# Kernel tuning notes

Hardware: AMD Instinct MI355X
Metric: run time of the kernel (lower is better)

The kernel has to match this reference:

```python
import jax, jax.numpy as jnp
import numpy as np

DIM = 2048
N_HEADS = 16
N_KV = 4
HEAD_DIM = DIM // N_HEADS  # 128
G = N_HEADS // N_KV        # queries per kv head
EPS = 1e-6
ROPE_BASE = 10000.0


def _rms_norm(x, w):
    # x: [..., head_dim]
    norm = jax.lax.rsqrt(jnp.mean(x * x, axis=-1, keepdims=True) + EPS)
    return x * norm * w


def _rope_tables(seq_len, dtype):
    inv_freq = 1.0 / (ROPE_BASE ** (jnp.arange(0, HEAD_DIM, 2, dtype=jnp.float32) / HEAD_DIM))
    t = jnp.arange(seq_len, dtype=jnp.float32)
    freqs = jnp.einsum('i,j->ij', t, inv_freq)          # [S, hd/2]
    emb = jnp.concatenate([freqs, freqs], axis=-1)       # [S, hd]
    return jnp.cos(emb).astype(dtype), jnp.sin(emb).astype(dtype)


def _rotate_half(x):
    x1, x2 = x[..., : HEAD_DIM // 2], x[..., HEAD_DIM // 2:]
    return jnp.concatenate([-x2, x1], axis=-1)


def setup_inputs() -> dict:
    key = jax.random.key(0)
    ks = jax.random.split(key, 7)
    x = jax.random.normal(ks[0], (2, 2048, DIM), dtype=jnp.float32)
    s = 0.02
    Wq = jax.random.normal(ks[1], (DIM, DIM), dtype=jnp.float32) * s
    Wk = jax.random.normal(ks[2], (DIM, N_KV * HEAD_DIM), dtype=jnp.float32) * s
    Wv = jax.random.normal(ks[3], (DIM, N_KV * HEAD_DIM), dtype=jnp.float32) * s
    Wo = jax.random.normal(ks[4], (DIM, DIM), dtype=jnp.float32) * s
    q_norm_w = jnp.ones((HEAD_DIM,), dtype=jnp.float32)
    k_norm_w = jnp.ones((HEAD_DIM,), dtype=jnp.float32)
    return {"x": x, "Wq": Wq, "Wk": Wk, "Wv": Wv, "Wo": Wo,
            "q_norm_w": q_norm_w, "k_norm_w": k_norm_w}


def reference(x, Wq, Wk, Wv, Wo, q_norm_w, k_norm_w):
    B, S, _ = x.shape
    q = (x @ Wq).reshape(B, S, N_HEADS, HEAD_DIM)
    k = (x @ Wk).reshape(B, S, N_KV, HEAD_DIM)
    v = (x @ Wv).reshape(B, S, N_KV, HEAD_DIM)

    q = _rms_norm(q, q_norm_w)
    k = _rms_norm(k, k_norm_w)

    q = q.transpose(0, 2, 1, 3)  # [B, H, S, hd]
    k = k.transpose(0, 2, 1, 3)  # [B, KV, S, hd]
    v = v.transpose(0, 2, 1, 3)

    cos, sin = _rope_tables(S, x.dtype)  # [S, hd], broadcasts over B,H
    q = q * cos + _rotate_half(q) * sin
    k = k * cos + _rotate_half(k) * sin

    # GQA: group queries by kv head instead of repeating K/V (same math as repeat_interleave)
    qg = q.reshape(B, N_KV, G, S, HEAD_DIM)
    scale = HEAD_DIM ** -0.5
    scores = jnp.einsum('bkgqd,bkkd2->bkgqk2'.replace('k2', 'K').replace('d2', 'd'),
                        qg, k) if False else jnp.einsum('bkgqd,bkKd->bkgqK', qg, k) * scale
    attn = jax.nn.softmax(scores, axis=-1)               # [B, KV, G, S, S]
    out = jnp.einsum('bkgqK,bkKd->bkgqd', attn, v)       # [B, KV, G, S, hd]
    out = out.reshape(B, N_HEADS, S, HEAD_DIM).transpose(0, 2, 1, 3).reshape(B, S, DIM)
    return out @ Wo
```

## Files before the change

### kernel.cpp

```cpp
#include <hip/hip_runtime.h>
#include <stdint.h>

#define LOG2E 1.4426950408889634f

typedef __attribute__((ext_vector_type(8))) short short8;
typedef __attribute__((ext_vector_type(4))) float floatx4;
typedef unsigned int u32;

__device__ __forceinline__ float bf2f(unsigned short h) {
  union { unsigned int u; float f; } v; v.u = ((unsigned int)h) << 16; return v.f;
}
__device__ __forceinline__ unsigned short f2bf(float f) {
  union { float f; unsigned int u; } v; v.f = f;
  unsigned int r = v.u + 0x7FFFu + ((v.u >> 16) & 1u);
  return (unsigned short)(r >> 16);
}
__device__ __forceinline__ u32 fbits(float f) {
  union { float f; u32 u; } v; v.f = f; return v.u;
}
__device__ __forceinline__ void async16(void* lds, const void* g) {
  __builtin_amdgcn_global_load_lds((const __attribute__((address_space(1))) u32*)g,
                                   (__attribute__((address_space(3))) u32*)lds, 16, 0, 0);
}

__global__ __launch_bounds__(256) void cvt_f32_bf16(const float* __restrict__ src,
                                                    unsigned short* __restrict__ dst, int n) {
  int i = (blockIdx.x * 256 + threadIdx.x) * 8;
  if (i >= n) return;
  float4 a = ((const float4*)(src + i))[0];
  float4 b = ((const float4*)(src + i))[1];
  union { uint4 v; unsigned short u[8]; } o;
  o.u[0] = f2bf(a.x); o.u[1] = f2bf(a.y); o.u[2] = f2bf(a.z); o.u[3] = f2bf(a.w);
  o.u[4] = f2bf(b.x); o.u[5] = f2bf(b.y); o.u[6] = f2bf(b.z); o.u[7] = f2bf(b.w);
  *(uint4*)(dst + i) = o.v;
}

__global__ __launch_bounds__(256) void transpose_cvt4(const float* __restrict__ Wq,
                                                      const float* __restrict__ Wk,
                                                      const float* __restrict__ Wv,
                                                      const float* __restrict__ Wo,
                                                      unsigned short* __restrict__ WTqkv,
                                                      unsigned short* __restrict__ WoT) {
  const int R = 2048;
  int bid = blockIdx.x;
  const float* src; unsigned short* dst; int C;
  if (bid < 1024) { src = Wq; dst = WTqkv; C = 2048; }
  else if (bid < 1280) { src = Wk; dst = WTqkv + (size_t)2048 * 2048; C = 512; bid -= 1024; }
  else if (bid < 1536) { src = Wv; dst = WTqkv + (size_t)2048 * 2048 + (size_t)512 * 2048; C = 512; bid -= 1280; }
  else { src = Wo; dst = WoT; C = 2048; bid -= 1536; }

  __shared__ unsigned short tile[64][65];
  int tc = C >> 6;
  int br = bid / tc, bc = bid % tc;
  int r0 = br << 6, c0 = bc << 6;
  int i = threadIdx.x >> 2, cc = (threadIdx.x & 3) << 4;
  const float4* g = (const float4*)(src + (size_t)(r0 + i) * C + c0 + cc);
  float4 f0 = g[0], f1 = g[1], f2 = g[2], f3 = g[3];
  unsigned short u[16];
  u[0]=f2bf(f0.x); u[1]=f2bf(f0.y); u[2]=f2bf(f0.z); u[3]=f2bf(f0.w);
  u[4]=f2bf(f1.x); u[5]=f2bf(f1.y); u[6]=f2bf(f1.z); u[7]=f2bf(f1.w);
  u[8]=f2bf(f2.x); u[9]=f2bf(f2.y); u[10]=f2bf(f2.z); u[11]=f2bf(f2.w);
  u[12]=f2bf(f3.x); u[13]=f2bf(f3.y); u[14]=f2bf(f3.z); u[15]=f2bf(f3.w);
#pragma unroll
  for (int j = 0; j < 16; ++j) tile[i][cc + j] = u[j];
  __syncthreads();
  union { uint4 v[2]; unsigned short u[16]; } buf;
#pragma unroll
  for (int j = 0; j < 16; ++j) buf.u[j] = tile[cc + j][i];
  uint4* o = (uint4*)(dst + (size_t)(c0 + i) * R + r0 + cc);
  o[0] = buf.v[0]; o[1] = buf.v[1];
}

template <typename OutT>
__global__ __launch_bounds__(256) void gemm_nt(const unsigned short* __restrict__ A,
                                               const unsigned short* __restrict__ BT,
                                               OutT* __restrict__ C,
                                               int M, int N, int K) {
  __shared__ unsigned short As[2][128 * 32];
  __shared__ unsigned short Bs[2][128 * 32];
  const int nb = N >> 7;
  const int bm = blockIdx.x / nb, bn = blockIdx.x % nb;
  const int m0 = bm << 7, n0 = bn << 7;
  const int tid = threadIdx.x;
  const int lane = tid & 63, wave = tid >> 6;
  const int l15 = lane & 15, quad = lane >> 4;
  const int wm = (wave >> 1) << 6, wn = (wave & 1) << 6;

  floatx4 acc[4][4];
#pragma unroll
  for (int i = 0; i < 4; ++i)
#pragma unroll
    for (int j = 0; j < 4; ++j) acc[i][j] = (floatx4){0.f, 0.f, 0.f, 0.f};

  const int Lc0 = wave * 128 + lane;
#pragma unroll 1
  for (int pre = 0; pre < 1; ++pre) {
#pragma unroll
    for (int i = 0; i < 2; ++i) {
      int Lc = Lc0 + i * 64;
      int row = Lc >> 2;
      int c = (lane & 3) ^ ((row >> 1) & 3);
      async16(As[0] + (size_t)Lc * 8, A + (size_t)(m0 + row) * K + c * 8);
      async16(Bs[0] + (size_t)Lc * 8, BT + (size_t)(n0 + row) * K + c * 8);
    }
  }

  const int nk = K >> 5;
  for (int it = 0; it < nk; ++it) {
    const int cur = it & 1;
    __syncthreads();
    if (it + 1 < nk) {
      int k1 = (it + 1) << 5;
#pragma unroll
      for (int i = 0; i < 2; ++i) {
        int Lc = Lc0 + i * 64;
        int row = Lc >> 2;
        int c = (lane & 3) ^ ((row >> 1) & 3);
        async16(As[cur ^ 1] + (size_t)Lc * 8, A + (size_t)(m0 + row) * K + k1 + c * 8);
        async16(Bs[cur ^ 1] + (size_t)Lc * 8, BT + (size_t)(n0 + row) * K + k1 + c * 8);
      }
    }
    short8 af[4], bf[4];
#pragma unroll
    for (int mt = 0; mt < 4; ++mt) {
      int m = wm + mt * 16 + l15;
      af[mt] = *(const short8*)(&As[cur][(m * 4 + (quad ^ ((m >> 1) & 3))) * 8]);
    }
#pragma unroll
    for (int nt = 0; nt < 4; ++nt) {
      int n = wn + nt * 16 + l15;
      bf[nt] = *(const short8*)(&Bs[cur][(n * 4 + (quad ^ ((n >> 1) & 3))) * 8]);
    }
#pragma unroll
    for (int mt = 0; mt < 4; ++mt)
#pragma unroll
      for (int nt = 0; nt < 4; ++nt)
        acc[mt][nt] = __builtin_amdgcn_mfma_f32_16x16x32_bf16(af[mt], bf[nt], acc[mt][nt], 0, 0, 0);
  }
#pragma unroll
  for (int mt = 0; mt < 4; ++mt)
#pragma unroll
    for (int nt = 0; nt < 4; ++nt)
#pragma unroll
      for (int r = 0; r < 4; ++r) {
        int m = m0 + wm + mt * 16 + quad * 4 + r;
        int n = n0 + wn + nt * 16 + l15;
        float v = acc[mt][nt][r];
        if constexpr (sizeof(OutT) == 2)
          C[(size_t)m * N + n] = (OutT)f2bf(v);
        else
          C[(size_t)m * N + n] = (OutT)v;
      }
}

__global__ __launch_bounds__(256) void norm_rope(const unsigned short* __restrict__ qkv,
                                                 const float* __restrict__ qw,
                                                 const float* __restrict__ kw,
                                                 unsigned short* __restrict__ qT,
                                                 unsigned short* __restrict__ kT) {
  const int S = 2048;
  int wid = blockIdx.x * 4 + (threadIdx.x >> 6);
  int lane = threadIdx.x & 63;
  int slot = wid % 20;
  int bs = wid / 20;
  int s = bs & (S - 1), b = bs >> 11;
  const unsigned short* src;
  unsigned short* dst;
  const float* w;
  float scale;
  if (slot < 16) {
    src = qkv + (size_t)bs * 3072 + slot * 128;
    dst = qT + ((size_t)(b * 16 + slot) * S + s) * 128;
    w = qw; scale = 0.08838834764831845f * 1.4426950408889634f;
  } else {
    int kvi = slot - 16;
    src = qkv + (size_t)bs * 3072 + 2048 + kvi * 128;
    dst = kT + ((size_t)(b * 4 + kvi) * S + s) * 128;
    w = kw; scale = 1.0f;
  }
  float x1 = bf2f(src[lane]), x2 = bf2f(src[lane + 64]);
  float ss = x1 * x1 + x2 * x2;
#pragma unroll
  for (int m = 1; m < 64; m <<= 1) ss += __shfl_xor(ss, m, 64);
  float rms = rsqrtf(ss * (1.0f / 128.0f) + 1e-6f);
  float y1 = x1 * rms * w[lane];
  float y2 = x2 * rms * w[lane + 64];
  float ang = (float)s * exp2f((float)lane * -0.2076205059304601f);
  float c = cosf(ang), sn = sinf(ang);
  float o1 = (y1 * c - y2 * sn) * scale;
  float o2 = (y2 * c + y1 * sn) * scale;
  dst[lane] = f2bf(o1);
  dst[lane + 64] = f2bf(o2);
}

__global__ __launch_bounds__(256) void v_transpose(const unsigned short* __restrict__ qkv,
                                                   unsigned short* __restrict__ vT) {
  const int S = 2048;
  int bid = blockIdx.x;
  int dt = bid & 1, st = (bid >> 1) & 31, kv = (bid >> 6) & 3, b = bid >> 8;
  int s0 = st << 6, d0 = dt << 6;
  __shared__ unsigned short tile[64][65];
  int i = threadIdx.x >> 2, cc = (threadIdx.x & 3) << 4;
  union { uint4 v[2]; unsigned short u[16]; } buf;
  const uint4* g = (const uint4*)(qkv + ((size_t)(b * S) + s0 + i) * 3072 + 2560 + kv * 128 + d0 + cc);
  buf.v[0] = g[0]; buf.v[1] = g[1];
#pragma unroll
  for (int j = 0; j < 16; ++j) tile[i][cc + j] = buf.u[j];
  __syncthreads();
#pragma unroll
  for (int j = 0; j < 16; ++j) buf.u[j] = tile[cc + j][i];
  uint4* o = (uint4*)(vT + ((size_t)(b * 4 + kv) * 128 + d0 + i) * S + s0 + cc);
  o[0] = buf.v[0]; o[1] = buf.v[1];
}

__global__ __launch_bounds__(256, 2) void flash_attn(const unsigned short* __restrict__ qT,
                                                     const unsigned short* __restrict__ kT,
                                                     const unsigned short* __restrict__ vT,
                                                     unsigned short* __restrict__ ao) {
  const int S = 2048;
  int bid = blockIdx.x;
  int qt = bid & 15, h = (bid >> 4) & 15, b = bid >> 8;
  int kv = h >> 2;
  int tid = threadIdx.x;
  int lane = tid & 63, wave = tid >> 6;
  int l15 = lane & 15, quad = lane >> 4;

  __shared__ unsigned short Ks[2][64 * 128];
  __shared__ unsigned short VTs[2][128 * 64];
  __shared__ unsigned short Ps[4][32 * 64];
  unsigned short* Psw = Ps[wave];

  short8 bq[2][4];
  const unsigned short* qbase = qT + ((size_t)(b * 16 + h) * S + qt * 128 + wave * 32) * 128;
#pragma unroll
  for (int nt = 0; nt < 2; ++nt)
#pragma unroll
    for (int kk = 0; kk < 4; ++kk)
      bq[nt][kk] = *(const short8*)(qbase + (size_t)(nt * 16 + l15) * 128 + kk * 32 + quad * 8);

  floatx4 O[2][8];
#pragma unroll
  for (int mt = 0; mt < 2; ++mt)
#pragma unroll
    for (int dt = 0; dt < 8; ++dt) O[mt][dt] = (floatx4){0.f, 0.f, 0.f, 0.f};
  float l_acc[2] = {0.f, 0.f};

  const size_t kbase = (size_t)(b * 4 + kv) * S * 128;
  const size_t vbase = (size_t)(b * 4 + kv) * 128 * S;

#pragma unroll
  for (int i = 0; i < 4; ++i) {
    int Lc = (wave * 4 + i) * 64 + lane;
    int row = Lc >> 4, cjk = (lane & 15) ^ (row & 7);
    async16(Ks[0] + (size_t)Lc * 8, kT + kbase + (size_t)row * 128 + cjk * 8);
    int d = Lc >> 3, cjv = (lane & 7) ^ (d & 7);
    async16(VTs[0] + (size_t)Lc * 8, vT + vbase + (size_t)d * S + cjv * 8);
  }

  for (int kt = 0; kt < 32; ++kt) {
    int cur = kt & 1;
    __syncthreads();
    if (kt + 1 < 32) {
#pragma unroll
      for (int i = 0; i < 4; ++i) {
        int Lc = (wave * 4 + i) * 64 + lane;
        int row = Lc >> 4, cjk = (lane & 15) ^ (row & 7);
        async16(Ks[cur ^ 1] + (size_t)Lc * 8,
                kT + kbase + (size_t)((kt + 1) * 64 + row) * 128 + cjk * 8);
        int d = Lc >> 3, cjv = (lane & 7) ^ (d & 7);
        async16(VTs[cur ^ 1] + (size_t)Lc * 8,
                vT + vbase + (size_t)d * S + (kt + 1) * 64 + cjv * 8);
      }
    }

    floatx4 st[4][2];
#pragma unroll
    for (int a = 0; a < 4; ++a)
#pragma unroll
      for (int nt = 0; nt < 2; ++nt) st[a][nt] = (floatx4){0.f, 0.f, 0.f, 0.f};
#pragma unroll
    for (int kk = 0; kk < 4; ++kk)
#pragma unroll
      for (int a = 0; a < 4; ++a) {
        int m = a * 16 + l15;
        short8 ak = *(const short8*)(&Ks[cur][(m * 16 + ((kk * 4 + quad) ^ (m & 7))) * 8]);
#pragma unroll
        for (int nt = 0; nt < 2; ++nt)
          st[a][nt] = __builtin_amdgcn_mfma_f32_16x16x32_bf16(ak, bq[nt][kk], st[a][nt], 0, 0, 0);
      }

#pragma unroll
    for (int nt = 0; nt < 2; ++nt) {
      int m = nt * 16 + l15;
#pragma unroll
      for (int a = 0; a < 4; ++a) {
        float e0 = __builtin_amdgcn_exp2f(st[a][nt][0]);
        float e1 = __builtin_amdgcn_exp2f(st[a][nt][1]);
        float e2 = __builtin_amdgcn_exp2f(st[a][nt][2]);
        float e3 = __builtin_amdgcn_exp2f(st[a][nt][3]);
        l_acc[nt] += (e0 + e1) + (e2 + e3);
        u32 p01 = __builtin_amdgcn_perm(fbits(e1) + 0x8000u, fbits(e0) + 0x8000u, 0x07060302u);
        u32 p23 = __builtin_amdgcn_perm(fbits(e3) + 0x8000u, fbits(e2) + 0x8000u, 0x07060302u);
        int c = (a * 2 + (quad >> 1)) ^ (m & 7);
        uint2 pk; pk.x = p01; pk.y = p23;
        *(uint2*)(&Psw[(m * 8 + c) * 8 + (quad & 1) * 4]) = pk;
      }
    }

#pragma unroll
    for (int kk2 = 0; kk2 < 2; ++kk2) {
      short8 ap[2];
#pragma unroll
      for (int mt = 0; mt < 2; ++mt) {
        int m = mt * 16 + l15;
        ap[mt] = *(const short8*)(&Psw[(m * 8 + ((kk2 * 4 + quad) ^ (m & 7))) * 8]);
      }
#pragma unroll
      for (int dt = 0; dt < 8; ++dt) {
        int n = dt * 16 + l15;
        short8 bv = *(const short8*)(&VTs[cur][(n * 8 + ((kk2 * 4 + quad) ^ (n & 7))) * 8]);
#pragma unroll
        for (int mt = 0; mt < 2; ++mt)
          O[mt][dt] = __builtin_amdgcn_mfma_f32_16x16x32_bf16(ap[mt], bv, O[mt][dt], 0, 0, 0);
      }
    }
  }

  float linv[2];
#pragma unroll
  for (int nt = 0; nt < 2; ++nt) {
    float l = l_acc[nt];
    l += __shfl_xor(l, 16, 64);
    l += __shfl_xor(l, 32, 64);
    linv[nt] = 1.f / l;
  }
#pragma unroll
  for (int mt = 0; mt < 2; ++mt)
#pragma unroll
    for (int r = 0; r < 4; ++r) {
      float inv = __shfl(linv[mt], quad * 4 + r, 64);
      int s = qt * 128 + wave * 32 + mt * 16 + quad * 4 + r;
#pragma unroll
      for (int dt = 0; dt < 8; ++dt) {
        int d = dt * 16 + l15;
        ao[((size_t)(b * S + s) * 16 + h) * 128 + d] = f2bf(O[mt][dt][r] * inv);
      }
    }
}

extern "C" void kernel_launch(void* const* d_in, const int* in_sizes, int n_in,
                              void* d_out, int out_size, void* d_ws, size_t ws_size,
                              hipStream_t stream) {
  const float* x  = (const float*)d_in[0];
  const float* Wq = (const float*)d_in[1];
  const float* Wk = (const float*)d_in[2];
  const float* Wv = (const float*)d_in[3];
  const float* Wo = (const float*)d_in[4];
  const float* qw = (const float*)d_in[5];
  const float* kw = (const float*)d_in[6];
  float* out = (float*)d_out;

  unsigned short* p = (unsigned short*)d_ws;
  unsigned short* xbf   = p; p += (size_t)4096 * 2048;
  unsigned short* WTqkv = p; p += (size_t)3072 * 2048;
  unsigned short* WoT   = p; p += (size_t)2048 * 2048;
  unsigned short* qkv   = p; p += (size_t)4096 * 3072;
  unsigned short* qTb   = p; p += (size_t)2 * 16 * 2048 * 128;
  unsigned short* kTb   = p; p += (size_t)2 * 4 * 2048 * 128;
  unsigned short* vTb   = p; p += (size_t)2 * 4 * 2048 * 128;
  unsigned short* ao    = p; p += (size_t)4096 * 2048;

  cvt_f32_bf16<<<4096, 256, 0, stream>>>(x, xbf, 4096 * 2048);
  transpose_cvt4<<<2560, 256, 0, stream>>>(Wq, Wk, Wv, Wo, WTqkv, WoT);

  gemm_nt<unsigned short><<<768, 256, 0, stream>>>(xbf, WTqkv, qkv, 4096, 3072, 2048);

  norm_rope<<<20480, 256, 0, stream>>>(qkv, qw, kw, qTb, kTb);
  v_transpose<<<512, 256, 0, stream>>>(qkv, vTb);

  flash_attn<<<512, 256, 0, stream>>>(qTb, kTb, vTb, ao);

  gemm_nt<float><<<512, 256, 0, stream>>>(ao, WoT, out, 4096, 2048, 2048);
}
```

Baseline: 325.2 us.

## Add 256x256-tile pipelined GEMM for QKV projection and raise MFMA priority in attention

Replaces the 128x128 QKV projection GEMM with a 256x256-tile, 512-thread kernel. It uses a two-buffer, four-phase async LDS pipeline with explicit vmcnt/lgkmcnt waits, s_setprio around MFMA bursts, and an XCD-aware block remap. The larger tiles are meant to raise data reuse per LDS load and overlap global loads with MFMA. The flash attention kernel also gets s_setprio around its MFMA loops. In exchange, only 192 workgroups are launched, which may underfill the 256 CUs, and the hand-written wait counts are fragile.

```diff
diff --git a/kernel.cpp b/kernel.cpp
--- a/kernel.cpp
+++ b/kernel.cpp
@@ -93,16 +93,13 @@
     for (int j = 0; j < 4; ++j) acc[i][j] = (floatx4){0.f, 0.f, 0.f, 0.f};
 
   const int Lc0 = wave * 128 + lane;
-#pragma unroll 1
-  for (int pre = 0; pre < 1; ++pre) {
-#pragma unroll
-    for (int i = 0; i < 2; ++i) {
-      int Lc = Lc0 + i * 64;
-      int row = Lc >> 2;
-      int c = (lane & 3) ^ ((row >> 1) & 3);
-      async16(As[0] + (size_t)Lc * 8, A + (size_t)(m0 + row) * K + c * 8);
-      async16(Bs[0] + (size_t)Lc * 8, BT + (size_t)(n0 + row) * K + c * 8);
-    }
+#pragma unroll
+  for (int i = 0; i < 2; ++i) {
+    int Lc = Lc0 + i * 64;
+    int row = Lc >> 2;
+    int c = (lane & 3) ^ ((row >> 1) & 3);
+    async16(As[0] + (size_t)Lc * 8, A + (size_t)(m0 + row) * K + c * 8);
+    async16(Bs[0] + (size_t)Lc * 8, BT + (size_t)(n0 + row) * K + c * 8);
   }
 
   const int nk = K >> 5;
@@ -146,6 +143,153 @@
         int m = m0 + wm + mt * 16 + quad * 4 + r;
         int n = n0 + wn + nt * 16 + l15;
         float v = acc[mt][nt][r];
+        if constexpr (sizeof(OutT) == 2)
+          C[(size_t)m * N + n] = (OutT)f2bf(v);
+        else
+          C[(size_t)m * N + n] = (OutT)v;
+      }
+}
+
+template <typename OutT>
+__global__ __launch_bounds__(512, 2) void gemm_nt_256(const unsigned short* __restrict__ A,
+                                                      const unsigned short* __restrict__ BT,
+                                                      OutT* __restrict__ C,
+                                                      int M, int N, int K) {
+  (void)M;
+  __shared__ unsigned short As[2][16384];
+  __shared__ unsigned short Bs[2][16384];
+  const int nbn = N >> 8;
+  const int nwg = gridDim.x;
+  int wg = blockIdx.x;
+  {
+    int cpx = nwg >> 3;
+    wg = (wg & 7) * cpx + (wg >> 3);
+  }
+  const int m0 = (wg / nbn) << 8;
+  const int n0 = (wg % nbn) << 8;
+  const int tid = threadIdx.x;
+  const int lane = tid & 63, wave = tid >> 6;
+  const int l15 = lane & 15, quad = lane >> 4;
+  const int wr = wave >> 2, wc = wave & 3;
+  const int rA = wr * 128 + l15;
+  const int rB = wc * 64 + l15;
+
+  floatx4 acc[8][4];
+#pragma unroll
+  for (int i = 0; i < 8; ++i)
+#pragma unroll
+    for (int j = 0; j < 4; ++j) acc[i][j] = (floatx4){0.f, 0.f, 0.f, 0.f};
+
+  const unsigned short* Ag = A + (size_t)m0 * K;
+  const unsigned short* Bg = BT + (size_t)n0 * K;
+
+  auto STAGE = [&](unsigned short* dst, const unsigned short* g) {
+#pragma unroll
+    for (int j = 0; j < 2; ++j) {
+      int idx = j * 512 + tid;
+      int r = idx >> 2;
+      int c = (idx & 3) ^ (r & 3);
+      async16(dst + (size_t)idx * 8, g + (size_t)r * K + c * 8);
+    }
+  };
+  auto RD = [&](const unsigned short* buf, int row, int ch) -> short8 {
+    int kh = ch >> 2;
+    int cq = (ch & 3) ^ (row & 3);
+    return *(const short8*)(buf + kh * 8192 + row * 32 + cq * 8);
+  };
+
+#define BAR() __builtin_amdgcn_s_barrier()
+#define LGKM0() do { asm volatile("s_waitcnt lgkmcnt(0)" ::: "memory"); \
+                     __builtin_amdgcn_sched_barrier(0); } while (0)
+
+  STAGE(As[0], Ag);
+  STAGE(Bs[0], Bg);
+  STAGE(As[0] + 8192, Ag + 32);
+  STAGE(Bs[0] + 8192, Bg + 32);
+  STAGE(As[1], Ag + 64);
+  STAGE(Bs[1], Bg + 64);
+  STAGE(As[1] + 8192, Ag + 96);
+  asm volatile("s_waitcnt vmcnt(6)" ::: "memory");
+  BAR();
+
+  short8 af[8], bfr[4];
+  const int NT = K >> 6;
+  for (int t = 0; t < NT; ++t) {
+    unsigned short* Ac = As[t & 1];
+    unsigned short* Bc = Bs[t & 1];
+    unsigned short* Bn = Bs[(t & 1) ^ 1];
+    const unsigned short* Agt = Ag + (size_t)(t + 2) * 64;
+    const unsigned short* Bgt = Bg + (size_t)(t + 2) * 64;
+
+#pragma unroll
+    for (int mf = 0; mf < 8; ++mf) af[mf] = RD(Ac, rA + mf * 16, quad);
+#pragma unroll
+    for (int nf = 0; nf < 4; ++nf) bfr[nf] = RD(Bc, rB + nf * 16, quad);
+    if (t + 1 < NT) STAGE(Bn + 8192, Bg + (size_t)(t + 1) * 64 + 32);
+    BAR(); LGKM0();
+    __builtin_amdgcn_s_setprio(1);
+#pragma unroll
+    for (int mf = 0; mf < 4; ++mf)
+#pragma unroll
+      for (int nf = 0; nf < 4; ++nf)
+        acc[mf][nf] = __builtin_amdgcn_mfma_f32_16x16x32_bf16(af[mf], bfr[nf], acc[mf][nf], 0, 0, 0);
+    __builtin_amdgcn_s_setprio(0);
+    BAR();
+
+    if (t + 2 < NT) STAGE(Ac, Agt);
+    BAR(); LGKM0();
+    __builtin_amdgcn_s_setprio(1);
+#pragma unroll
+    for (int mf = 4; mf < 8; ++mf)
+#pragma unroll
+      for (int nf = 0; nf < 4; ++nf)
+        acc[mf][nf] = __builtin_amdgcn_mfma_f32_16x16x32_bf16(af[mf], bfr[nf], acc[mf][nf], 0, 0, 0);
+    __builtin_amdgcn_s_setprio(0);
+    BAR();
+
+#pragma unroll
+    for (int mf = 0; mf < 8; ++mf) af[mf] = RD(Ac, rA + mf * 16, 4 + quad);
+#pragma unroll
+    for (int nf = 0; nf < 4; ++nf) bfr[nf] = RD(Bc, rB + nf * 16, 4 + quad);
+    if (t + 2 < NT) STAGE(Bc, Bgt);
+    BAR(); LGKM0();
+    __builtin_amdgcn_s_setprio(1);
+#pragma unroll
+    for (int mf = 0; mf < 4; ++mf)
+#pragma unroll
+      for (int nf = 0; nf < 4; ++nf)
+        acc[mf][nf] = __builtin_amdgcn_mfma_f32_16x16x32_bf16(af[mf], bfr[nf], acc[mf][nf], 0, 0, 0);
+    __builtin_amdgcn_s_setprio(0);
+    BAR();
+
+    if (t + 2 < NT) STAGE(Ac + 8192, Agt + 32);
+    if (t + 2 < NT) {
+      asm volatile("s_waitcnt vmcnt(6)" ::: "memory");
+    } else if (t + 1 < NT) {
+      asm volatile("s_waitcnt vmcnt(0)" ::: "memory");
+    }
+    BAR(); LGKM0();
+    __builtin_amdgcn_s_setprio(1);
+#pragma unroll
+    for (int mf = 4; mf < 8; ++mf)
+#pragma unroll
+      for (int nf = 0; nf < 4; ++nf)
+        acc[mf][nf] = __builtin_amdgcn_mfma_f32_16x16x32_bf16(af[mf], bfr[nf], acc[mf][nf], 0, 0, 0);
+    __builtin_amdgcn_s_setprio(0);
+    BAR();
+  }
+#undef BAR
+#undef LGKM0
+
+#pragma unroll
+  for (int mf = 0; mf < 8; ++mf)
+#pragma unroll
+    for (int nf = 0; nf < 4; ++nf)
+#pragma unroll
+      for (int r = 0; r < 4; ++r) {
+        int m = m0 + wr * 128 + mf * 16 + quad * 4 + r;
+        int n = n0 + wc * 64 + nf * 16 + l15;
+        float v = acc[mf][nf][r];
         if constexpr (sizeof(OutT) == 2)
           C[(size_t)m * N + n] = (OutT)f2bf(v);
         else
@@ -278,6 +422,7 @@
     for (int a = 0; a < 4; ++a)
 #pragma unroll
       for (int nt = 0; nt < 2; ++nt) st[a][nt] = (floatx4){0.f, 0.f, 0.f, 0.f};
+    __builtin_amdgcn_s_setprio(1);
 #pragma unroll
     for (int kk = 0; kk < 4; ++kk)
 #pragma unroll
@@ -288,6 +433,7 @@
         for (int nt = 0; nt < 2; ++nt)
           st[a][nt] = __builtin_amdgcn_mfma_f32_16x16x32_bf16(ak, bq[nt][kk], st[a][nt], 0, 0, 0);
       }
+    __builtin_amdgcn_s_setprio(0);
 
 #pragma unroll
     for (int nt = 0; nt < 2; ++nt) {
@@ -307,6 +453,7 @@
       }
     }
 
+    __builtin_amdgcn_s_setprio(1);
 #pragma unroll
     for (int kk2 = 0; kk2 < 2; ++kk2) {
       short8 ap[2];
@@ -324,6 +471,7 @@
           O[mt][dt] = __builtin_amdgcn_mfma_f32_16x16x32_bf16(ap[mt], bv, O[mt][dt], 0, 0, 0);
       }
     }
+    __builtin_amdgcn_s_setprio(0);
   }
 
   float linv[2];
@@ -373,7 +521,7 @@
   cvt_f32_bf16<<<4096, 256, 0, stream>>>(x, xbf, 4096 * 2048);
   transpose_cvt4<<<2560, 256, 0, stream>>>(Wq, Wk, Wv, Wo, WTqkv, WoT);
 
-  gemm_nt<unsigned short><<<768, 256, 0, stream>>>(xbf, WTqkv, qkv, 4096, 3072, 2048);
+  gemm_nt_256<unsigned short><<<192, 512, 0, stream>>>(xbf, WTqkv, qkv, 4096, 3072, 2048);
 
   norm_rope<<<20480, 256, 0, stream>>>(qkv, qw, kw, qTb, kTb);
   v_transpose<<<512, 256, 0, stream>>>(qkv, vTb);
```

New measurement: 329.1 us. Within noise of the previous version (+1.2%).
